# Optimization experiments

Hardware: AMD Instinct MI355X
Metric: run time of the kernel (lower is better)

## Reference

```python
import jax, jax.numpy as jnp
import numpy as np
from jax import lax

N = 100000   # num_nodes
E = 1600000  # num_edges (avg degree 16)
F = 128      # num_features
H = 256      # hidden_channels
C = 64       # num_classes
K = 10       # propagation steps
ALPHA = 0.1
BETA = 0.5
THETA = 0.5
EPS = 1e-5   # BatchNorm eps


def setup_inputs() -> dict:
    key = jax.random.key(0)
    ks = jax.random.split(key, 16)
    x = jax.random.normal(ks[0], (N, F), dtype=jnp.float32)
    src = jax.random.randint(ks[1], (E,), 0, N, dtype=jnp.int32)
    dst = jax.random.randint(ks[2], (E,), 0, N, dtype=jnp.int32)
    # row-normalized adjacency weights so repeated A@z stays bounded
    deg = jax.ops.segment_sum(jnp.ones((E,), jnp.float32), dst, num_segments=N)
    w = (1.0 / jnp.maximum(deg, 1.0))[dst]
    # MLP params (Linear + BatchNorm per hidden layer)
    W1 = jax.random.normal(ks[3], (F, H), dtype=jnp.float32) * 0.05
    b1 = jnp.zeros((H,), jnp.float32)
    g1 = jnp.ones((H,), jnp.float32)
    be1 = jnp.zeros((H,), jnp.float32)
    W2 = jax.random.normal(ks[4], (H, H), dtype=jnp.float32) * 0.05
    b2 = jnp.zeros((H,), jnp.float32)
    g2 = jnp.ones((H,), jnp.float32)
    be2 = jnp.zeros((H,), jnp.float32)
    W3 = jax.random.normal(ks[5], (H, C), dtype=jnp.float32) * 0.05
    b3 = jnp.zeros((C,), jnp.float32)
    # lazy caches (warm-start memories); nonzero so the blend branch is taken
    z_sam = jax.random.normal(ks[6], (N, C), dtype=jnp.float32) * 0.1
    g_sam = jax.random.normal(ks[7], (N, C), dtype=jnp.float32) * 0.01
    return dict(x=x, src=src, dst=dst, w=w,
                W1=W1, b1=b1, g1=g1, be1=be1,
                W2=W2, b2=b2, g2=g2, be2=be2,
                W3=W3, b3=b3, z_sam=z_sam, g_sam=g_sam, size=N)


def _bn(h, gamma, beta):
    # BatchNorm1d in training mode: batch statistics over nodes
    mu = jnp.mean(h, axis=0)
    var = jnp.var(h, axis=0)
    return (h - mu) * jax.lax.rsqrt(var + EPS) * gamma + beta


def reference(x, src, dst, w, W1, b1, g1, be1, W2, b2, g2, be2, W3, b3,
              z_sam, g_sam, size):
    # MLP stack: Linear -> BN -> ReLU (dropout omitted: deterministic reference)
    h = jax.nn.relu(_bn(x @ W1 + b1, g1, be1))
    h = jax.nn.relu(_bn(h @ W2 + b2, g2, be2))
    logits = h @ W3 + b3  # [N, C]

    def spmm(z):
        # (A @ z)_i = sum_{j -> i} w_ij * z_j
        return jax.ops.segment_sum(z[src] * w[:, None], dst, num_segments=N)

    # Lazy_Prop.forward: warm-start blend, then K propagation steps
    use_x = jnp.all(z_sam[:size] == 0.0)
    z0 = jnp.where(use_x, logits, (1.0 - BETA) * z_sam + BETA * logits)
    z = lax.fori_loop(0, K, lambda i, z: (1.0 - ALPHA) * spmm(z) + ALPHA * logits, z0)
    return jax.nn.log_softmax(z, axis=1)
```

## Files before the change

### kernel.cpp

```cpp
#include <hip/hip_runtime.h>
#include <hip/hip_bf16.h>

#define NODES 100000
#define EDGES 1600000
#define FEAT  128
#define HID   256
#define CLS   64
#define KPROP 10
#define ALPHA_C 0.1f
#define BETA_C  0.5f
#define BN_EPS  1e-5f

typedef __attribute__((ext_vector_type(8))) short short8;
typedef __attribute__((ext_vector_type(4))) float f32x4;

static __device__ __forceinline__ unsigned short f2b(float f) {
    __hip_bfloat16 h = __float2bfloat16(f);
    return *(unsigned short*)&h;
}
static __device__ __forceinline__ float b2f(unsigned short u) {
    __hip_bfloat16 h;
    *(unsigned short*)&h = u;
    return __bfloat162float(h);
}
static __device__ __forceinline__ float asf(unsigned int u) {
    union { unsigned int u; float f; } c; c.u = u; return c.f;
}

__global__ void packwt_k(const float* __restrict__ W, unsigned short* __restrict__ Wt,
                         int K, int N)
{
    int i = blockIdx.x * 256 + threadIdx.x;
    if (i < K * N) {
        int k = i / N, n = i - k * N;
        Wt[(size_t)n * K + k] = f2b(W[i]);
    }
}

__global__ void xcvt_k(const float* __restrict__ x, unsigned short* __restrict__ xb)
{
    int i = blockIdx.x * 256 + threadIdx.x;
    if (i < NODES * FEAT / 8) {
        float4 a = ((const float4*)x)[2 * i];
        float4 b = ((const float4*)x)[2 * i + 1];
        short8 o;
        o[0] = (short)f2b(a.x); o[1] = (short)f2b(a.y);
        o[2] = (short)f2b(a.z); o[3] = (short)f2b(a.w);
        o[4] = (short)f2b(b.x); o[5] = (short)f2b(b.y);
        o[6] = (short)f2b(b.z); o[7] = (short)f2b(b.w);
        ((short8*)xb)[i] = o;
    }
}

__global__ __launch_bounds__(256, 2)
void gemm1_k(const unsigned short* __restrict__ xb, const unsigned short* __restrict__ Wt,
             const float* __restrict__ bias, unsigned short* __restrict__ h1,
             float* __restrict__ gsum, float* __restrict__ gsq,
             int M, int nchunks, int nblk)
{
    __shared__ unsigned short Blds[256 * FEAT];
    const int lane = threadIdx.x & 63;
    const int wv   = threadIdx.x >> 6;
    const int quad = lane >> 4;
    const int l16  = lane & 15;
    const int colbase = wv * 64;

    #pragma unroll
    for (int i0 = 0; i0 < 4096; i0 += 256) {
        int i  = i0 + threadIdx.x;
        int c  = i >> 4;
        int k8 = i & 15;
        short8 v = *(const short8*)(Wt + (size_t)c * FEAT + k8 * 8);
        int byte = c * 256 + ((k8 * 16) ^ ((c & 7) << 4));
        *(short8*)((char*)Blds + byte) = v;
    }
    __syncthreads();

    float bcol[4];
    #pragma unroll
    for (int ct = 0; ct < 4; ++ct) bcol[ct] = bias[colbase + ct * 16 + l16];
    float ps[4] = {0.f, 0.f, 0.f, 0.f};
    float pq[4] = {0.f, 0.f, 0.f, 0.f};

    short8 ah0[2][4], ah1[2][4];

#define LOAD1(AH, CHK)                                                         \
    if ((CHK) < nchunks) {                                                     \
        const int rb_ = (CHK) * 32;                                            \
        _Pragma("unroll")                                                      \
        for (int rt = 0; rt < 2; ++rt) {                                       \
            const int row_ = rb_ + rt * 16 + l16;                              \
            const unsigned short* ap_ = xb + (size_t)row_ * FEAT + quad * 8;   \
            _Pragma("unroll")                                                  \
            for (int ks = 0; ks < 4; ++ks)                                     \
                AH[rt][ks] = *(const short8*)(ap_ + ks * 32);                  \
        }                                                                      \
    }

#define COMP1(AH, CHK)                                                         \
    {                                                                          \
        const int rb_ = (CHK) * 32;                                            \
        f32x4 acc[2][4];                                                       \
        _Pragma("unroll")                                                      \
        for (int i = 0; i < 2; ++i)                                            \
            _Pragma("unroll")                                                  \
            for (int j = 0; j < 4; ++j)                                        \
                acc[i][j] = (f32x4){0.f, 0.f, 0.f, 0.f};                       \
        _Pragma("unroll")                                                      \
        for (int ks = 0; ks < 4; ++ks) {                                       \
            _Pragma("unroll")                                                  \
            for (int ct = 0; ct < 4; ++ct) {                                   \
                const int col_ = colbase + ct * 16 + l16;                      \
                const int boff = col_ * 256                                    \
                               + ((ks * 64 + quad * 16) ^ ((col_ & 7) << 4));  \
                short8 bf = *(const short8*)((const char*)Blds + boff);        \
                acc[0][ct] = __builtin_amdgcn_mfma_f32_16x16x32_bf16(AH[0][ks], bf, acc[0][ct], 0, 0, 0); \
                acc[1][ct] = __builtin_amdgcn_mfma_f32_16x16x32_bf16(AH[1][ks], bf, acc[1][ct], 0, 0, 0); \
            }                                                                  \
        }                                                                      \
        _Pragma("unroll")                                                      \
        for (int ct = 0; ct < 4; ++ct) {                                       \
            const int col_ = colbase + ct * 16 + l16;                          \
            _Pragma("unroll")                                                  \
            for (int rt = 0; rt < 2; ++rt) {                                   \
                _Pragma("unroll")                                              \
                for (int r2 = 0; r2 < 4; ++r2) {                               \
                    const int row_ = rb_ + rt * 16 + quad * 4 + r2;            \
                    if (row_ < M) {                                            \
                        float vv = acc[rt][ct][r2] + bcol[ct];                 \
                        ps[ct] += vv; pq[ct] += vv * vv;                       \
                        h1[(size_t)row_ * HID + col_] = f2b(vv);               \
                    }                                                          \
                }                                                              \
            }                                                                  \
        }                                                                      \
    }

    int chunk = blockIdx.x;
    LOAD1(ah0, chunk)
    while (chunk < nchunks) {
        const int cn1 = chunk + nblk;
        LOAD1(ah1, cn1)
        __builtin_amdgcn_sched_barrier(0);
        COMP1(ah0, chunk)
        chunk = cn1;
        if (chunk >= nchunks) break;
        const int cn2 = chunk + nblk;
        LOAD1(ah0, cn2)
        __builtin_amdgcn_sched_barrier(0);
        COMP1(ah1, chunk)
        chunk = cn2;
    }
#undef LOAD1
#undef COMP1

    #pragma unroll
    for (int ct = 0; ct < 4; ++ct) {
        float s = ps[ct];
        s += __shfl_xor(s, 16, 64);
        s += __shfl_xor(s, 32, 64);
        float q = pq[ct];
        q += __shfl_xor(q, 16, 64);
        q += __shfl_xor(q, 32, 64);
        if (lane < 16) {
            atomicAdd(&gsum[colbase + ct * 16 + lane], s);
            atomicAdd(&gsq[colbase + ct * 16 + lane], q);
        }
    }
}

template<bool FUSE, bool STATS, bool OUTF32, int KK, int NCOLG, int COLS>
__global__ __launch_bounds__(256, 2)
void gemm_lds_k(const unsigned short* __restrict__ Ain, const unsigned short* __restrict__ Wt,
                const float* __restrict__ bias,
                const float* __restrict__ scale, const float* __restrict__ shift,
                void* __restrict__ outp,
                float* __restrict__ gsum, float* __restrict__ gsq,
                int M, int N, int nchunks, int nblk)
{
    constexpr int NK8 = KK / 32;
    constexpr int NKH = NK8 / 2;
    constexpr int CHROWS = (COLS == 128) ? 64 : 128;
    __shared__ unsigned short Blds[COLS * KK];
    __shared__ float Slds[KK];
    __shared__ float Hlds[KK];

    const int lane = threadIdx.x & 63;
    const int wv   = threadIdx.x >> 6;
    const int quad = lane >> 4;
    const int l16  = lane & 15;
    const int colg = (NCOLG > 1) ? (blockIdx.x % NCOLG) : 0;
    const int blk0 = (NCOLG > 1) ? (blockIdx.x / NCOLG) : blockIdx.x;
    const int colpan = colg * COLS;
    const int lwcol  = (COLS == 128) ? (wv & 1) * 64 : 0;
    const int rwoff  = (COLS == 128) ? (wv >> 1) * 32 : wv * 32;

    {
        const unsigned short* wp = Wt + (size_t)colpan * KK;
        constexpr int ELEMS = COLS * KK / 8;
        #pragma unroll
        for (int i0 = 0; i0 < ELEMS; i0 += 256) {
            int i  = i0 + threadIdx.x;
            int c  = i / (KK / 8);
            int k8 = i - c * (KK / 8);
            short8 v = *(const short8*)(wp + (size_t)c * KK + k8 * 8);
            int byte = c * (KK * 2) + ((k8 * 16) ^ ((c & 7) << 4));
            *(short8*)((char*)Blds + byte) = v;
        }
        if constexpr (FUSE) {
            for (int i = threadIdx.x; i < KK; i += 256) {
                Slds[i] = scale[i];
                Hlds[i] = shift[i];
            }
        }
    }
    __syncthreads();

    float bcol[4];
    #pragma unroll
    for (int ct = 0; ct < 4; ++ct) bcol[ct] = bias[colpan + lwcol + ct * 16 + l16];

    float ps[4] = {0.f, 0.f, 0.f, 0.f};
    float pq[4] = {0.f, 0.f, 0.f, 0.f};

    short8 hb0[2][NKH], hb1[2][NKH];
    f32x4 acc[2][4];

#define LOADH(B, CHK, H)                                                       \
    if ((CHK) < nchunks) {                                                     \
        const int rb_ = (CHK) * CHROWS + rwoff;                                \
        _Pragma("unroll")                                                      \
        for (int rt = 0; rt < 2; ++rt) {                                       \
            const int row_ = rb_ + rt * 16 + l16;                              \
            const unsigned short* ap_ = Ain + (size_t)row_ * KK                \
                                        + (H) * NKH * 32 + quad * 8;           \
            _Pragma("unroll")                                                  \
            for (int ks = 0; ks < NKH; ++ks)                                   \
                B[rt][ks] = *(const short8*)(ap_ + ks * 32);                   \
        }                                                                      \
    }

#define COMPH(B, H)                                                            \
    {                                                                          \
        _Pragma("unroll")                                                      \
        for (int ks = 0; ks < NKH; ++ks) {                                     \
            const int gks = (H) * NKH + ks;                                    \
            const int k_ = gks * 32 + quad * 8;                                \
            float sc[8], sh[8];                                                \
            if constexpr (FUSE) {                                              \
                float4 s0 = *(const float4*)&Slds[k_];                         \
                float4 s1 = *(const float4*)&Slds[k_ + 4];                     \
                float4 h0 = *(const float4*)&Hlds[k_];                         \
                float4 h1 = *(const float4*)&Hlds[k_ + 4];                     \
                sc[0]=s0.x; sc[1]=s0.y; sc[2]=s0.z; sc[3]=s0.w;                \
                sc[4]=s1.x; sc[5]=s1.y; sc[6]=s1.z; sc[7]=s1.w;                \
                sh[0]=h0.x; sh[1]=h0.y; sh[2]=h0.z; sh[3]=h0.w;                \
                sh[4]=h1.x; sh[5]=h1.y; sh[6]=h1.z; sh[7]=h1.w;                \
            }                                                                  \
            short8 a2[2];                                                      \
            _Pragma("unroll")                                                  \
            for (int rt = 0; rt < 2; ++rt) {                                   \
                if constexpr (FUSE) {                                          \
                    float v[8];                                                \
                    _Pragma("unroll")                                          \
                    for (int j = 0; j < 8; ++j)                                \
                        v[j] = b2f((unsigned short)B[rt][ks][j]);              \
                    _Pragma("unroll")                                          \
                    for (int j = 0; j < 8; ++j)                                \
                        v[j] = fmaxf(fmaf(v[j], sc[j], sh[j]), 0.f);           \
                    short8 av;                                                 \
                    _Pragma("unroll")                                          \
                    for (int j = 0; j < 8; ++j) av[j] = (short)f2b(v[j]);      \
                    a2[rt] = av;                                               \
                } else {                                                       \
                    a2[rt] = B[rt][ks];                                        \
                }                                                              \
            }                                                                  \
            _Pragma("unroll")                                                  \
            for (int ct = 0; ct < 4; ++ct) {                                   \
                const int lc_ = lwcol + ct * 16 + l16;                         \
                const int boff = lc_ * (KK * 2)                                \
                               + ((gks * 64 + quad * 16) ^ ((l16 & 7) << 4));  \
                short8 bf = *(const short8*)((const char*)Blds + boff);        \
                acc[0][ct] = __builtin_amdgcn_mfma_f32_16x16x32_bf16(a2[0], bf, acc[0][ct], 0, 0, 0); \
                acc[1][ct] = __builtin_amdgcn_mfma_f32_16x16x32_bf16(a2[1], bf, acc[1][ct], 0, 0, 0); \
            }                                                                  \
        }                                                                      \
    }

    int chunk = blk0;
    LOADH(hb0, chunk, 0)
    while (chunk < nchunks) {
        #pragma unroll
        for (int i = 0; i < 2; ++i)
            #pragma unroll
            for (int j = 0; j < 4; ++j)
                acc[i][j] = (f32x4){0.f, 0.f, 0.f, 0.f};

        LOADH(hb1, chunk, 1)
        __builtin_amdgcn_sched_barrier(0);
        COMPH(hb0, 0)
        const int nxt = chunk + nblk;
        LOADH(hb0, nxt, 0)
        __builtin_amdgcn_sched_barrier(0);
        COMPH(hb1, 1)

        const int rb_ = chunk * CHROWS + rwoff;
        #pragma unroll
        for (int ct = 0; ct < 4; ++ct) {
            const int col_ = colpan + lwcol + ct * 16 + l16;
            #pragma unroll
            for (int rt = 0; rt < 2; ++rt) {
                #pragma unroll
                for (int r2 = 0; r2 < 4; ++r2) {
                    const int row_ = rb_ + rt * 16 + quad * 4 + r2;
                    if (row_ < M) {
                        float vv = acc[rt][ct][r2] + bcol[ct];
                        if constexpr (STATS) { ps[ct] += vv; pq[ct] += vv * vv; }
                        if constexpr (OUTF32) {
                            ((float*)outp)[(size_t)row_ * N + col_] = vv;
                        } else {
                            ((unsigned short*)outp)[(size_t)row_ * N + col_] = f2b(vv);
                        }
                    }
                }
            }
        }
        chunk = nxt;
    }
#undef LOADH
#undef COMPH

    if constexpr (STATS) {
        #pragma unroll
        for (int ct = 0; ct < 4; ++ct) {
            float s = ps[ct];
            s += __shfl_xor(s, 16, 64);
            s += __shfl_xor(s, 32, 64);
            float q = pq[ct];
            q += __shfl_xor(q, 16, 64);
            q += __shfl_xor(q, 32, 64);
            if (lane < 16) {
                atomicAdd(&gsum[colpan + lwcol + ct * 16 + lane], s);
                atomicAdd(&gsq[colpan + lwcol + ct * 16 + lane], q);
            }
        }
    }
}

__global__ void bnfin_k(const float* __restrict__ sum, const float* __restrict__ sq,
                        const float* __restrict__ g, const float* __restrict__ be,
                        float* __restrict__ scale, float* __restrict__ shift)
{
    int c = threadIdx.x;
    float mu = sum[c] * (1.f / NODES);
    float var = sq[c] * (1.f / NODES) - mu * mu;
    float sc = g[c] * rsqrtf(var + BN_EPS);
    scale[c] = sc;
    shift[c] = be[c] - mu * sc;
}

__global__ void flag_k(const float* __restrict__ zs, int* __restrict__ flag)
{
    int i = blockIdx.x * 256 + threadIdx.x;
    bool nz = (i < NODES * CLS) && (zs[i] != 0.f);
    if (__any(nz)) {
        if ((threadIdx.x & 63) == 0) *flag = 1;
    }
}

__global__ void blend_k(const float* __restrict__ zs, const float* __restrict__ logits,
                        const int* __restrict__ flag, unsigned short* __restrict__ z0)
{
    int i = blockIdx.x * 256 + threadIdx.x;
    if (i < NODES * CLS) {
        float l = logits[i];
        float v = (*flag) ? ((1.f - BETA_C) * zs[i] + BETA_C * l) : l;
        z0[i] = f2b(v);
    }
}

__global__ void count_k(const int* __restrict__ dst, int* __restrict__ cntx)
{
    int t = blockIdx.x * 256 + threadIdx.x;
    if (t >= EDGES / 4) return;
    int4 d = ((const int4*)dst)[t];
    int* c = cntx + (size_t)(blockIdx.x & 7) * NODES;
    atomicAdd(&c[d.x], 1);
    atomicAdd(&c[d.y], 1);
    atomicAdd(&c[d.z], 1);
    atomicAdd(&c[d.w], 1);
}

__global__ void sumoff_k(int* __restrict__ cntx, int* __restrict__ cnt)
{
    int n = blockIdx.x * 256 + threadIdx.x;
    if (n >= NODES) return;
    int tot = 0;
    int p[8];
    #pragma unroll
    for (int x = 0; x < 8; ++x) {
        p[x] = tot;
        tot += cntx[(size_t)x * NODES + n];
    }
    #pragma unroll
    for (int x = 0; x < 8; ++x)
        cntx[(size_t)x * NODES + n] = p[x];
    cnt[n] = tot;
}

__global__ void scan1_k(const int* __restrict__ cnt, int* __restrict__ rowptr,
                        int* __restrict__ bsum)
{
    __shared__ int s[256];
    int tid = threadIdx.x;
    int i = blockIdx.x * 256 + tid;
    int v = (i < NODES) ? cnt[i] : 0;
    s[tid] = v;
    __syncthreads();
    for (int off = 1; off < 256; off <<= 1) {
        int t = (tid >= off) ? s[tid - off] : 0;
        __syncthreads();
        s[tid] += t;
        __syncthreads();
    }
    if (i < NODES) rowptr[i] = s[tid] - v;
    if (tid == 255) bsum[blockIdx.x] = s[255];
}

__global__ void scan2_k(const int* __restrict__ bsum, int* __restrict__ boffs, int nb)
{
    __shared__ int s[512];
    int tid = threadIdx.x;
    int v = (tid < nb) ? bsum[tid] : 0;
    s[tid] = v;
    __syncthreads();
    for (int off = 1; off < 512; off <<= 1) {
        int t = (tid >= off) ? s[tid - off] : 0;
        __syncthreads();
        s[tid] += t;
        __syncthreads();
    }
    if (tid < nb) boffs[tid] = s[tid] - v;
}

__global__ void scan3_k(int* __restrict__ rowptr, const int* __restrict__ boffs,
                        const int* __restrict__ cntx, int* __restrict__ curx)
{
    int i = blockIdx.x * 256 + threadIdx.x;
    if (i < NODES) {
        int v = rowptr[i] + boffs[blockIdx.x];
        rowptr[i] = v;
        #pragma unroll
        for (int x = 0; x < 8; ++x)
            curx[(size_t)x * NODES + i] = v + cntx[(size_t)x * NODES + i];
    }
    if (i == 0) rowptr[NODES] = EDGES;
}

__global__ void posfill_k(const int* __restrict__ dst, int* __restrict__ curx,
                          int* __restrict__ pos)
{
    int t = blockIdx.x * 256 + threadIdx.x;
    if (t >= EDGES / 4) return;
    int4 d = ((const int4*)dst)[t];
    int* cur = curx + (size_t)(blockIdx.x & 7) * NODES;
    int4 p;
    p.x = atomicAdd(&cur[d.x], 1);
    p.y = atomicAdd(&cur[d.y], 1);
    p.z = atomicAdd(&cur[d.z], 1);
    p.w = atomicAdd(&cur[d.w], 1);
    ((int4*)pos)[t] = p;
}

__global__ void scat_k(const int* __restrict__ src, const int* __restrict__ pos,
                       int* __restrict__ esrc)
{
    int e = blockIdx.x * 256 + threadIdx.x;
    if (e < EDGES) esrc[pos[e]] = src[e];
}

__global__ __launch_bounds__(256)
void prop_k(const int* __restrict__ rowptr, const int* __restrict__ esrc,
            const unsigned long long* __restrict__ zin, const float* __restrict__ logits,
            uint4* __restrict__ zout)
{
    int row = blockIdx.x * 32 + (threadIdx.x >> 3);
    if (row >= NODES) return;
    int l8 = threadIdx.x & 7;
    int beg = rowptr[row], end = rowptr[row + 1];
    float a0 = 0.f, a1 = 0.f, a2 = 0.f, a3 = 0.f;
    float a4 = 0.f, a5 = 0.f, a6 = 0.f, a7 = 0.f;

    for (int cbeg = beg; cbeg < end; cbeg += 16) {
        int e0 = cbeg + l8, e1 = cbeg + 8 + l8;
        int s0 = (e0 < end) ? esrc[e0] : 0;
        int s1 = (e1 < end) ? esrc[e1] : 0;
        int cnt = min(16, end - cbeg);
        if (cnt == 16) {
            int idx[16];
            #pragma unroll
            for (int u = 0; u < 8; ++u) idx[u] = __shfl(s0, u, 8);
            #pragma unroll
            for (int u = 0; u < 8; ++u) idx[8 + u] = __shfl(s1, u, 8);
            unsigned long long vv[32];
            #pragma unroll
            for (int u = 0; u < 16; ++u) {
                const unsigned long long* p = zin + (size_t)idx[u] * 16 + l8 * 2;
                vv[2 * u]     = __hip_atomic_load(p,     __ATOMIC_RELAXED, __HIP_MEMORY_SCOPE_AGENT);
                vv[2 * u + 1] = __hip_atomic_load(p + 1, __ATOMIC_RELAXED, __HIP_MEMORY_SCOPE_AGENT);
            }
            #pragma unroll
            for (int u = 0; u < 16; ++u) {
                unsigned int x0 = (unsigned int)vv[2 * u];
                unsigned int x1 = (unsigned int)(vv[2 * u] >> 32);
                unsigned int x2 = (unsigned int)vv[2 * u + 1];
                unsigned int x3 = (unsigned int)(vv[2 * u + 1] >> 32);
                a0 += asf(x0 << 16);  a1 += asf(x0 & 0xffff0000u);
                a2 += asf(x1 << 16);  a3 += asf(x1 & 0xffff0000u);
                a4 += asf(x2 << 16);  a5 += asf(x2 & 0xffff0000u);
                a6 += asf(x3 << 16);  a7 += asf(x3 & 0xffff0000u);
            }
        } else {
            for (int j = 0; j < cnt; ++j) {
                int sv = (j < 8) ? __shfl(s0, j, 8) : __shfl(s1, j - 8, 8);
                const unsigned long long* p = zin + (size_t)sv * 16 + l8 * 2;
                unsigned long long v0 = __hip_atomic_load(p,     __ATOMIC_RELAXED, __HIP_MEMORY_SCOPE_AGENT);
                unsigned long long v1 = __hip_atomic_load(p + 1, __ATOMIC_RELAXED, __HIP_MEMORY_SCOPE_AGENT);
                unsigned int x0 = (unsigned int)v0;
                unsigned int x1 = (unsigned int)(v0 >> 32);
                unsigned int x2 = (unsigned int)v1;
                unsigned int x3 = (unsigned int)(v1 >> 32);
                a0 += asf(x0 << 16);  a1 += asf(x0 & 0xffff0000u);
                a2 += asf(x1 << 16);  a3 += asf(x1 & 0xffff0000u);
                a4 += asf(x2 << 16);  a5 += asf(x2 & 0xffff0000u);
                a6 += asf(x3 << 16);  a7 += asf(x3 & 0xffff0000u);
            }
        }
    }
    float dg = (float)(end - beg);
    float inv = 1.f / fmaxf(dg, 1.f);
    float cc = (1.f - ALPHA_C) * inv;
    const float* lp = logits + (size_t)row * CLS + l8 * 8;
    float4 lv0 = *(const float4*)lp;
    float4 lv1 = *(const float4*)(lp + 4);
    float r0 = cc * a0 + ALPHA_C * lv0.x;
    float r1 = cc * a1 + ALPHA_C * lv0.y;
    float r2 = cc * a2 + ALPHA_C * lv0.z;
    float r3 = cc * a3 + ALPHA_C * lv0.w;
    float r4 = cc * a4 + ALPHA_C * lv1.x;
    float r5 = cc * a5 + ALPHA_C * lv1.y;
    float r6 = cc * a6 + ALPHA_C * lv1.z;
    float r7 = cc * a7 + ALPHA_C * lv1.w;
    uint4 w;
    w.x = ((unsigned int)f2b(r1) << 16) | (unsigned int)f2b(r0);
    w.y = ((unsigned int)f2b(r3) << 16) | (unsigned int)f2b(r2);
    w.z = ((unsigned int)f2b(r5) << 16) | (unsigned int)f2b(r4);
    w.w = ((unsigned int)f2b(r7) << 16) | (unsigned int)f2b(r6);
    zout[(size_t)row * 8 + l8] = w;
}

__global__ __launch_bounds__(256)
void logsoftmax_k(const unsigned short* __restrict__ z, float* __restrict__ out)
{
    int row = blockIdx.x * 4 + (threadIdx.x >> 6);
    if (row >= NODES) return;
    int lane = threadIdx.x & 63;
    float v = b2f(z[(size_t)row * CLS + lane]);
    float m = v;
    #pragma unroll
    for (int off = 32; off > 0; off >>= 1) m = fmaxf(m, __shfl_xor(m, off, 64));
    float ex = expf(v - m);
    float s = ex;
    #pragma unroll
    for (int off = 32; off > 0; off >>= 1) s += __shfl_xor(s, off, 64);
    out[(size_t)row * CLS + lane] = (v - m) - logf(s);
}

extern "C" void kernel_launch(void* const* d_in, const int* in_sizes, int n_in,
                              void* d_out, int out_size, void* d_ws, size_t ws_size,
                              hipStream_t stream)
{
    const float* x   = (const float*)d_in[0];
    const int*   src = (const int*)d_in[1];
    const int*   dst = (const int*)d_in[2];
    const float* W1  = (const float*)d_in[4];
    const float* b1  = (const float*)d_in[5];
    const float* g1  = (const float*)d_in[6];
    const float* be1 = (const float*)d_in[7];
    const float* W2  = (const float*)d_in[8];
    const float* b2  = (const float*)d_in[9];
    const float* g2  = (const float*)d_in[10];
    const float* be2 = (const float*)d_in[11];
    const float* W3  = (const float*)d_in[12];
    const float* b3  = (const float*)d_in[13];
    const float* zsam = (const float*)d_in[14];
    float* outp = (float*)d_out;

    const int NPAD = NODES + 128;
    uint8_t* base = (uint8_t*)d_ws;
    float* s_scale1 = (float*)(base);
    float* s_shift1 = s_scale1 + 256;
    float* s_scale2 = s_shift1 + 256;
    float* s_shift2 = s_scale2 + 256;
    float* s_sum    = s_shift2 + 256;
    float* s_sq     = s_sum + 256;
    int*   flag     = (int*)(s_sq + 256);

    unsigned short* Wt1 = (unsigned short*)(base + (1 << 14));
    unsigned short* Wt2 = Wt1 + (size_t)FEAT * HID;
    unsigned short* Wt3 = Wt2 + (size_t)HID * HID;
    unsigned short* h1  = Wt3 + (size_t)HID * CLS;
    unsigned short* h2  = h1 + (size_t)NPAD * HID;
    float* logits = (float*)(h2 + (size_t)NPAD * HID);
    unsigned short* zA  = (unsigned short*)(logits + (size_t)NODES * CLS);
    unsigned short* zB  = zA + (size_t)NODES * CLS;
    int* esrc   = (int*)(zB + (size_t)NODES * CLS);
    int* cntx   = esrc + EDGES;
    int* curx   = cntx + (size_t)8 * NODES;
    int* rowptr = curx + (size_t)8 * NODES;
    int* cnt    = rowptr + (NODES + 1);
    int* bsum   = cnt + NODES;
    int* boffs  = bsum + 512;
    int* pos = (int*)h1;
    unsigned short* xb = h2;

    const int NCHUNK2 = (NODES + 63) / 64;
    const int NBLK2   = (NCHUNK2 + 1) / 2;
    const int NCHUNK3 = (NODES + 127) / 128;
    const int NBLK3   = (NCHUNK3 + 1) / 2;
    const int NCH1    = (NODES + 31) / 32;
    const int NB1     = 512;
    const int SCANB   = (NODES + 255) / 256;
    const int EB4     = (EDGES / 4 + 255) / 256;

    packwt_k<<<(FEAT * HID + 255) / 256, 256, 0, stream>>>(W1, Wt1, FEAT, HID);
    packwt_k<<<(HID * HID + 255) / 256, 256, 0, stream>>>(W2, Wt2, HID, HID);
    packwt_k<<<(HID * CLS + 255) / 256, 256, 0, stream>>>(W3, Wt3, HID, CLS);
    xcvt_k<<<(NODES * FEAT / 8 + 255) / 256, 256, 0, stream>>>(x, xb);
    hipMemsetAsync(h1 + (size_t)NODES * HID, 0, 128 * HID * sizeof(unsigned short), stream);
    hipMemsetAsync(xb + (size_t)NODES * FEAT, 0, 128 * FEAT * sizeof(unsigned short), stream);

    hipMemsetAsync(cntx, 0, (size_t)8 * NODES * sizeof(int), stream);
    count_k<<<EB4, 256, 0, stream>>>(dst, cntx);
    sumoff_k<<<SCANB, 256, 0, stream>>>(cntx, cnt);
    scan1_k<<<SCANB, 256, 0, stream>>>(cnt, rowptr, bsum);
    scan2_k<<<1, 512, 0, stream>>>(bsum, boffs, SCANB);
    scan3_k<<<SCANB, 256, 0, stream>>>(rowptr, boffs, cntx, curx);
    posfill_k<<<EB4, 256, 0, stream>>>(dst, curx, pos);
    scat_k<<<EDGES / 256, 256, 0, stream>>>(src, pos, esrc);

    hipMemsetAsync(s_sum, 0, 512 * sizeof(float), stream);
    gemm1_k<<<NB1, 256, 0, stream>>>(xb, Wt1, b1, h1, s_sum, s_sq, NODES, NCH1, NB1);
    bnfin_k<<<1, 256, 0, stream>>>(s_sum, s_sq, g1, be1, s_scale1, s_shift1);

    hipMemsetAsync(s_sum, 0, 512 * sizeof(float), stream);
    gemm_lds_k<true, true, false, HID, 2, 128><<<NBLK2 * 2, 256, 0, stream>>>(
        h1, Wt2, b2, s_scale1, s_shift1, h2, s_sum, s_sq, NODES, HID, NCHUNK2, NBLK2);
    bnfin_k<<<1, 256, 0, stream>>>(s_sum, s_sq, g2, be2, s_scale2, s_shift2);
    hipMemsetAsync(h2 + (size_t)NODES * HID, 0, 128 * HID * sizeof(unsigned short), stream);

    gemm_lds_k<true, false, true, HID, 1, 64><<<NBLK3, 256, 0, stream>>>(
        h2, Wt3, b3, s_scale2, s_shift2, logits, nullptr, nullptr, NODES, CLS, NCHUNK3, NBLK3);

    hipMemsetAsync(flag, 0, sizeof(int), stream);
    flag_k<<<(NODES * CLS + 255) / 256, 256, 0, stream>>>(zsam, flag);
    blend_k<<<(NODES * CLS + 255) / 256, 256, 0, stream>>>(zsam, logits, flag, zA);

    const int PROPB = (NODES + 31) / 32;
    for (int it = 0; it < KPROP; ++it) {
        const unsigned long long* zi = (const unsigned long long*)((it & 1) ? zB : zA);
        uint4* zo = (uint4*)((it & 1) ? zA : zB);
        prop_k<<<PROPB, 256, 0, stream>>>(rowptr, esrc, zi, logits, zo);
    }

    logsoftmax_k<<<(NODES + 3) / 4, 256, 0, stream>>>(zA, outp);
}
```

Measured before the change: 870.0 us.

## Split propagation features into four 16-column panels to shrink gather working set

Stores the bf16 propagation state as four column panels of 16 features each, laid out panel-major, and processes each panel in a separate pass inside prop_k, with 4 lanes per row instead of 8. The aim is for the gathered working set of each pass (100k rows x 32 bytes) to fit better in cache, so random neighbour reads hit L2/MALL more often. In exchange, the edge index list and rowptr are re-read four times per step, and each gather moves 8 bytes instead of 16. Blend and log-softmax are updated to the new layout.

Measured after the change: 1.160 ms. +33.4%, slower.

```diff
diff --git a/kernel.cpp b/kernel.cpp
--- a/kernel.cpp
+++ b/kernel.cpp
@@ -376,7 +376,8 @@
     if (i < NODES * CLS) {
         float l = logits[i];
         float v = (*flag) ? ((1.f - BETA_C) * zs[i] + BETA_C * l) : l;
-        z0[i] = f2b(v);
+        int row = i >> 6, c = i & 63, p = c >> 4;
+        z0[((size_t)p * NODES + row) * 16 + (c & 15)] = f2b(v);
     }
 }
 
@@ -483,81 +484,71 @@
 __global__ __launch_bounds__(256)
 void prop_k(const int* __restrict__ rowptr, const int* __restrict__ esrc,
             const unsigned long long* __restrict__ zin, const float* __restrict__ logits,
-            uint4* __restrict__ zout)
-{
-    int row = blockIdx.x * 32 + (threadIdx.x >> 3);
+            unsigned long long* __restrict__ zout)
+{
+    int row = blockIdx.x * 64 + (threadIdx.x >> 2);
     if (row >= NODES) return;
-    int l8 = threadIdx.x & 7;
+    int l4 = threadIdx.x & 3;
     int beg = rowptr[row], end = rowptr[row + 1];
-    float a0 = 0.f, a1 = 0.f, a2 = 0.f, a3 = 0.f;
-    float a4 = 0.f, a5 = 0.f, a6 = 0.f, a7 = 0.f;
-
-    for (int cbeg = beg; cbeg < end; cbeg += 16) {
-        int e0 = cbeg + l8, e1 = cbeg + 8 + l8;
-        int s0 = (e0 < end) ? esrc[e0] : 0;
-        int s1 = (e1 < end) ? esrc[e1] : 0;
-        int cnt = min(16, end - cbeg);
-        if (cnt == 16) {
-            int idx[16];
-            #pragma unroll
-            for (int u = 0; u < 8; ++u) idx[u] = __shfl(s0, u, 8);
-            #pragma unroll
-            for (int u = 0; u < 8; ++u) idx[8 + u] = __shfl(s1, u, 8);
-            unsigned long long vv[32];
-            #pragma unroll
-            for (int u = 0; u < 16; ++u) {
-                const unsigned long long* p = zin + (size_t)idx[u] * 16 + l8 * 2;
-                vv[2 * u]     = __hip_atomic_load(p,     __ATOMIC_RELAXED, __HIP_MEMORY_SCOPE_AGENT);
-                vv[2 * u + 1] = __hip_atomic_load(p + 1, __ATOMIC_RELAXED, __HIP_MEMORY_SCOPE_AGENT);
-            }
-            #pragma unroll
-            for (int u = 0; u < 16; ++u) {
-                unsigned int x0 = (unsigned int)vv[2 * u];
-                unsigned int x1 = (unsigned int)(vv[2 * u] >> 32);
-                unsigned int x2 = (unsigned int)vv[2 * u + 1];
-                unsigned int x3 = (unsigned int)(vv[2 * u + 1] >> 32);
-                a0 += asf(x0 << 16);  a1 += asf(x0 & 0xffff0000u);
-                a2 += asf(x1 << 16);  a3 += asf(x1 & 0xffff0000u);
-                a4 += asf(x2 << 16);  a5 += asf(x2 & 0xffff0000u);
-                a6 += asf(x3 << 16);  a7 += asf(x3 & 0xffff0000u);
-            }
-        } else {
-            for (int j = 0; j < cnt; ++j) {
-                int sv = (j < 8) ? __shfl(s0, j, 8) : __shfl(s1, j - 8, 8);
-                const unsigned long long* p = zin + (size_t)sv * 16 + l8 * 2;
-                unsigned long long v0 = __hip_atomic_load(p,     __ATOMIC_RELAXED, __HIP_MEMORY_SCOPE_AGENT);
-                unsigned long long v1 = __hip_atomic_load(p + 1, __ATOMIC_RELAXED, __HIP_MEMORY_SCOPE_AGENT);
-                unsigned int x0 = (unsigned int)v0;
-                unsigned int x1 = (unsigned int)(v0 >> 32);
-                unsigned int x2 = (unsigned int)v1;
-                unsigned int x3 = (unsigned int)(v1 >> 32);
-                a0 += asf(x0 << 16);  a1 += asf(x0 & 0xffff0000u);
-                a2 += asf(x1 << 16);  a3 += asf(x1 & 0xffff0000u);
-                a4 += asf(x2 << 16);  a5 += asf(x2 & 0xffff0000u);
-                a6 += asf(x3 << 16);  a7 += asf(x3 & 0xffff0000u);
+    float dg = (float)(end - beg);
+    float cc = (1.f - ALPHA_C) / fmaxf(dg, 1.f);
+
+    #pragma unroll 1
+    for (int p = 0; p < 4; ++p) {
+        const unsigned long long* zp = zin + (size_t)p * NODES * 4;
+        float a0 = 0.f, a1 = 0.f, a2 = 0.f, a3 = 0.f;
+
+        for (int cbeg = beg; cbeg < end; cbeg += 16) {
+            int cnt = min(16, end - cbeg);
+            int eb = cbeg + l4 * 4;
+            int s0 = (eb     < end) ? esrc[eb]     : 0;
+            int s1 = (eb + 1 < end) ? esrc[eb + 1] : 0;
+            int s2 = (eb + 2 < end) ? esrc[eb + 2] : 0;
+            int s3 = (eb + 3 < end) ? esrc[eb + 3] : 0;
+            if (cnt == 16) {
+                int idx[16];
+                #pragma unroll
+                for (int j = 0; j < 16; ++j) {
+                    int sv = (j & 3) == 0 ? s0 : (j & 3) == 1 ? s1 : (j & 3) == 2 ? s2 : s3;
+                    idx[j] = __shfl(sv, j >> 2, 4);
+                }
+                unsigned long long vv[16];
+                #pragma unroll
+                for (int j = 0; j < 16; ++j)
+                    vv[j] = __hip_atomic_load(zp + (size_t)idx[j] * 4 + l4,
+                                              __ATOMIC_RELAXED, __HIP_MEMORY_SCOPE_AGENT);
+                #pragma unroll
+                for (int j = 0; j < 16; ++j) {
+                    unsigned int lo = (unsigned int)vv[j];
+                    unsigned int hi = (unsigned int)(vv[j] >> 32);
+                    a0 += asf(lo << 16);  a1 += asf(lo & 0xffff0000u);
+                    a2 += asf(hi << 16);  a3 += asf(hi & 0xffff0000u);
+                }
+            } else {
+                for (int j = 0; j < cnt; ++j) {
+                    int sv = (j & 3) == 0 ? s0 : (j & 3) == 1 ? s1 : (j & 3) == 2 ? s2 : s3;
+                    int id = __shfl(sv, j >> 2, 4);
+                    unsigned long long v = __hip_atomic_load(zp + (size_t)id * 4 + l4,
+                                                             __ATOMIC_RELAXED, __HIP_MEMORY_SCOPE_AGENT);
+                    unsigned int lo = (unsigned int)v;
+                    unsigned int hi = (unsigned int)(v >> 32);
+                    a0 += asf(lo << 16);  a1 += asf(lo & 0xffff0000u);
+                    a2 += asf(hi << 16);  a3 += asf(hi & 0xffff0000u);
+                }
             }
         }
-    }
-    float dg = (float)(end - beg);
-    float inv = 1.f / fmaxf(dg, 1.f);
-    float cc = (1.f - ALPHA_C) * inv;
-    const float* lp = logits + (size_t)row * CLS + l8 * 8;
-    float4 lv0 = *(const float4*)lp;
-    float4 lv1 = *(const float4*)(lp + 4);
-    float r0 = cc * a0 + ALPHA_C * lv0.x;
-    float r1 = cc * a1 + ALPHA_C * lv0.y;
-    float r2 = cc * a2 + ALPHA_C * lv0.z;
-    float r3 = cc * a3 + ALPHA_C * lv0.w;
-    float r4 = cc * a4 + ALPHA_C * lv1.x;
-    float r5 = cc * a5 + ALPHA_C * lv1.y;
-    float r6 = cc * a6 + ALPHA_C * lv1.z;
-    float r7 = cc * a7 + ALPHA_C * lv1.w;
-    uint4 w;
-    w.x = ((unsigned int)f2b(r1) << 16) | (unsigned int)f2b(r0);
-    w.y = ((unsigned int)f2b(r3) << 16) | (unsigned int)f2b(r2);
-    w.z = ((unsigned int)f2b(r5) << 16) | (unsigned int)f2b(r4);
-    w.w = ((unsigned int)f2b(r7) << 16) | (unsigned int)f2b(r6);
-    zout[(size_t)row * 8 + l8] = w;
+
+        const float* lp = logits + (size_t)row * CLS + p * 16 + l4 * 4;
+        float4 lv = *(const float4*)lp;
+        float r0 = cc * a0 + ALPHA_C * lv.x;
+        float r1 = cc * a1 + ALPHA_C * lv.y;
+        float r2 = cc * a2 + ALPHA_C * lv.z;
+        float r3 = cc * a3 + ALPHA_C * lv.w;
+        unsigned int w0 = ((unsigned int)f2b(r1) << 16) | (unsigned int)f2b(r0);
+        unsigned int w1 = ((unsigned int)f2b(r3) << 16) | (unsigned int)f2b(r2);
+        zout[(size_t)p * NODES * 4 + (size_t)row * 4 + l4] =
+            ((unsigned long long)w1 << 32) | w0;
+    }
 }
 
 __global__ __launch_bounds__(256)
@@ -566,7 +557,7 @@
     int row = blockIdx.x * 4 + (threadIdx.x >> 6);
     if (row >= NODES) return;
     int lane = threadIdx.x & 63;
-    float v = b2f(z[(size_t)row * CLS + lane]);
+    float v = b2f(z[((size_t)(lane >> 4) * NODES + row) * 16 + (lane & 15)]);
     float m = v;
     #pragma unroll
     for (int off = 32; off > 0; off >>= 1) m = fmaxf(m, __shfl_xor(m, off, 64));
@@ -667,10 +658,10 @@
     flag_k<<<(NODES * CLS + 255) / 256, 256, 0, stream>>>(zsam, flag);
     blend_k<<<(NODES * CLS + 255) / 256, 256, 0, stream>>>(zsam, logits, flag, zA);
 
-    const int PROPB = (NODES + 31) / 32;
+    const int PROPB = (NODES + 63) / 64;
     for (int it = 0; it < KPROP; ++it) {
         const unsigned long long* zi = (const unsigned long long*)((it & 1) ? zB : zA);
-        uint4* zo = (uint4*)((it & 1) ? zA : zB);
+        unsigned long long* zo = (unsigned long long*)((it & 1) ? zA : zB);
         prop_k<<<PROPB, 256, 0, stream>>>(rowptr, esrc, zi, logits, zo);
     }
 
```

## Replace second GEMM with persistent double-buffered kernel using direct global-to-LDS loads

Applied to the files above, without the earlier changes.

Adds a new persistent gemm2_k for the hidden-to-hidden layer. It uses 512-thread blocks and a fixed grid of 256 row groups times 2 column panels. Each block keeps its 128-column weight panel resident in swizzled LDS and streams 64-row A chunks into double-buffered LDS with global_load_lds, prefetching the next chunk while computing the current one. The aim is to hide global load latency and amortize the weight load across many chunks. The cost is a large LDS footprint that allows only one block per CU, and correctness depends on the swizzle and barrier ordering.

Result: no change. 861.8 us (-0.9%).

```diff
diff --git a/kernel.cpp b/kernel.cpp
--- a/kernel.cpp
+++ b/kernel.cpp
@@ -25,6 +25,11 @@
 }
 static __device__ __forceinline__ float asf(unsigned int u) {
     union { unsigned int u; float f; } c; c.u = u; return c.f;
+}
+static __device__ __forceinline__ void gl_lds16(const void* g, void* l) {
+    __builtin_amdgcn_global_load_lds(
+        (const __attribute__((address_space(1))) unsigned int*)g,
+        (__attribute__((address_space(3))) unsigned int*)l, 16, 0, 0);
 }
 
 __global__ void packwt_k(const float* __restrict__ W, unsigned short* __restrict__ Wt,
@@ -165,6 +170,146 @@
         if (lane < 16) {
             atomicAdd(&gsum[colbase + ct * 16 + lane], s);
             atomicAdd(&gsq[colbase + ct * 16 + lane], q);
+        }
+    }
+}
+
+__global__ __launch_bounds__(512, 1)
+void gemm2_k(const unsigned short* __restrict__ Ain, const unsigned short* __restrict__ Wt,
+             const float* __restrict__ bias,
+             const float* __restrict__ scale, const float* __restrict__ shift,
+             unsigned short* __restrict__ outp,
+             float* __restrict__ gsum, float* __restrict__ gsq,
+             int M, int nchunks, int nblk)
+{
+    __shared__ unsigned short Blds[128 * HID];
+    __shared__ unsigned short Alds[2][64 * HID];
+    __shared__ float Slds[HID];
+    __shared__ float Hlds[HID];
+
+    const int tid  = threadIdx.x;
+    const int lane = tid & 63;
+    const int wv   = tid >> 6;
+    const int quad = lane >> 4;
+    const int l16  = lane & 15;
+    const int ch   = wv & 1;
+    const int rg   = wv >> 1;
+    const int colg = blockIdx.x & 1;
+    const int blk0 = blockIdx.x >> 1;
+    const int colpan = colg * 128;
+
+    {
+        const unsigned short* wp = Wt + (size_t)colpan * HID;
+        #pragma unroll
+        for (int i0 = 0; i0 < 4096; i0 += 512) {
+            int i  = i0 + tid;
+            int c  = i >> 5;
+            int k8 = i & 31;
+            short8 v = *(const short8*)(wp + (size_t)c * HID + k8 * 8);
+            int byte = c * 512 + ((k8 * 16) ^ ((c & 7) << 4));
+            *(short8*)((char*)Blds + byte) = v;
+        }
+        if (tid < HID) { Slds[tid] = scale[tid]; Hlds[tid] = shift[tid]; }
+    }
+
+    float bcol[4];
+    #pragma unroll
+    for (int ct = 0; ct < 4; ++ct) bcol[ct] = bias[colpan + ch * 64 + ct * 16 + l16];
+    float ps[4] = {0.f, 0.f, 0.f, 0.f};
+    float pq[4] = {0.f, 0.f, 0.f, 0.f};
+
+#define STAGE2(BUF, CHK)                                                       \
+    if ((CHK) < nchunks) {                                                     \
+        const char* abase = (const char*)Ain + (size_t)(CHK) * 64 * 512;       \
+        char* lbase = (char*)Alds[BUF];                                        \
+        _Pragma("unroll")                                                      \
+        for (int j = 0; j < 4; ++j) {                                          \
+            const int P = j * 8192 + tid * 16;                                 \
+            const int L = P ^ (((P >> 9) & 7) << 4);                           \
+            gl_lds16(abase + L, lbase + P);                                    \
+        }                                                                      \
+    }
+
+#define COMP2(BUF, CHK)                                                        \
+    {                                                                          \
+        f32x4 acc[4];                                                          \
+        _Pragma("unroll")                                                      \
+        for (int j = 0; j < 4; ++j) acc[j] = (f32x4){0.f, 0.f, 0.f, 0.f};      \
+        const int row_l = rg * 16 + l16;                                       \
+        const char* albase = (const char*)Alds[BUF];                           \
+        _Pragma("unroll")                                                      \
+        for (int gks = 0; gks < 8; ++gks) {                                    \
+            const int k_ = gks * 32 + quad * 8;                                \
+            float4 s0 = *(const float4*)&Slds[k_];                             \
+            float4 s1 = *(const float4*)&Slds[k_ + 4];                         \
+            float4 h0 = *(const float4*)&Hlds[k_];                             \
+            float4 h1v = *(const float4*)&Hlds[k_ + 4];                        \
+            const int aoff = row_l * 512                                       \
+                           + ((gks * 64 + quad * 16) ^ ((row_l & 7) << 4));    \
+            short8 ar = *(const short8*)(albase + aoff);                       \
+            float v[8];                                                        \
+            _Pragma("unroll")                                                  \
+            for (int j = 0; j < 8; ++j) v[j] = b2f((unsigned short)ar[j]);     \
+            v[0] = fmaxf(fmaf(v[0], s0.x, h0.x), 0.f);                         \
+            v[1] = fmaxf(fmaf(v[1], s0.y, h0.y), 0.f);                         \
+            v[2] = fmaxf(fmaf(v[2], s0.z, h0.z), 0.f);                         \
+            v[3] = fmaxf(fmaf(v[3], s0.w, h0.w), 0.f);                         \
+            v[4] = fmaxf(fmaf(v[4], s1.x, h1v.x), 0.f);                        \
+            v[5] = fmaxf(fmaf(v[5], s1.y, h1v.y), 0.f);                        \
+            v[6] = fmaxf(fmaf(v[6], s1.z, h1v.z), 0.f);                        \
+            v[7] = fmaxf(fmaf(v[7], s1.w, h1v.w), 0.f);                        \
+            short8 a2;                                                         \
+            _Pragma("unroll")                                                  \
+            for (int j = 0; j < 8; ++j) a2[j] = (short)f2b(v[j]);              \
+            _Pragma("unroll")                                                  \
+            for (int ct = 0; ct < 4; ++ct) {                                   \
+                const int lc = ch * 64 + ct * 16 + l16;                        \
+                const int boff = lc * 512                                      \
+                               + ((gks * 64 + quad * 16) ^ ((l16 & 7) << 4));  \
+                short8 bf = *(const short8*)((const char*)Blds + boff);        \
+                acc[ct] = __builtin_amdgcn_mfma_f32_16x16x32_bf16(a2, bf, acc[ct], 0, 0, 0); \
+            }                                                                  \
+        }                                                                      \
+        const int rb_ = (CHK) * 64 + rg * 16;                                  \
+        _Pragma("unroll")                                                      \
+        for (int ct = 0; ct < 4; ++ct) {                                       \
+            const int col_ = colpan + ch * 64 + ct * 16 + l16;                 \
+            _Pragma("unroll")                                                  \
+            for (int r2 = 0; r2 < 4; ++r2) {                                   \
+                const int row_ = rb_ + quad * 4 + r2;                          \
+                if (row_ < M) {                                                \
+                    float vv = acc[ct][r2] + bcol[ct];                         \
+                    ps[ct] += vv; pq[ct] += vv * vv;                           \
+                    outp[(size_t)row_ * HID + col_] = f2b(vv);                 \
+                }                                                              \
+            }                                                                  \
+        }                                                                      \
+    }
+
+    int c = blk0, buf = 0;
+    STAGE2(0, c)
+    while (c < nchunks) {
+        __syncthreads();
+        const int cn = c + nblk;
+        if (buf == 0) { STAGE2(1, cn) } else { STAGE2(0, cn) }
+        COMP2(buf, c)
+        c = cn;
+        buf ^= 1;
+    }
+#undef STAGE2
+#undef COMP2
+
+    #pragma unroll
+    for (int ct = 0; ct < 4; ++ct) {
+        float s = ps[ct];
+        s += __shfl_xor(s, 16, 64);
+        s += __shfl_xor(s, 32, 64);
+        float q = pq[ct];
+        q += __shfl_xor(q, 16, 64);
+        q += __shfl_xor(q, 32, 64);
+        if (lane < 16) {
+            atomicAdd(&gsum[colpan + ch * 64 + ct * 16 + lane], s);
+            atomicAdd(&gsq[colpan + ch * 64 + ct * 16 + lane], q);
         }
     }
 }
@@ -626,7 +771,7 @@
     unsigned short* xb = h2;
 
     const int NCHUNK2 = (NODES + 63) / 64;
-    const int NBLK2   = (NCHUNK2 + 1) / 2;
+    const int NB2     = 256;
     const int NCHUNK3 = (NODES + 127) / 128;
     const int NBLK3   = (NCHUNK3 + 1) / 2;
     const int NCH1    = (NODES + 31) / 32;
@@ -655,8 +800,8 @@
     bnfin_k<<<1, 256, 0, stream>>>(s_sum, s_sq, g1, be1, s_scale1, s_shift1);
 
     hipMemsetAsync(s_sum, 0, 512 * sizeof(float), stream);
-    gemm_lds_k<true, true, false, HID, 2, 128><<<NBLK2 * 2, 256, 0, stream>>>(
-        h1, Wt2, b2, s_scale1, s_shift1, h2, s_sum, s_sq, NODES, HID, NCHUNK2, NBLK2);
+    gemm2_k<<<NB2 * 2, 512, 0, stream>>>(
+        h1, Wt2, b2, s_scale1, s_shift1, h2, s_sum, s_sq, NODES, NCHUNK2, NB2);
     bnfin_k<<<1, 256, 0, stream>>>(s_sum, s_sq, g2, be2, s_scale2, s_shift2);
     hipMemsetAsync(h2 + (size_t)NODES * HID, 0, 128 * HID * sizeof(unsigned short), stream);
 
```
